# Kernel optimization log

Hardware: AMD Instinct MI355X
Metric: run time of the kernel (lower is better)

Reference implementation:

```python
import jax, jax.numpy as jnp
import numpy as np

N_NODES = 50000
N_EDGES = 800000
IN_CH, HID_CH, OUT_CH = 512, 512, 256


def setup_inputs() -> dict:
    key = jax.random.key(0)
    ks = jax.random.split(key, 8)
    x = jax.random.normal(ks[0], (N_NODES, IN_CH), dtype=jnp.float32)
    edge_index = jax.random.randint(ks[1], (2, N_EDGES), 0, N_NODES, dtype=jnp.int32)
    def glorot(k, fan_in, fan_out):
        s = jnp.sqrt(6.0 / (fan_in + fan_out))
        return jax.random.uniform(k, (fan_in, fan_out), jnp.float32, -s, s)
    W1 = glorot(ks[2], IN_CH, HID_CH)
    b1 = jnp.zeros((HID_CH,), jnp.float32)
    W2 = glorot(ks[3], HID_CH, HID_CH)
    b2 = jnp.zeros((HID_CH,), jnp.float32)
    W3 = glorot(ks[4], HID_CH, OUT_CH)
    b3 = jnp.zeros((OUT_CH,), jnp.float32)
    return {"x": x, "edge_index": edge_index, "W1": W1, "b1": b1,
            "W2": W2, "b2": b2, "W3": W3, "b3": b3}


def _gcn_conv(x, src, dst, W, b, n_nodes):
    """PyG GCNConv: add self-loops, symmetric deg^-1/2 normalization,
    linear transform, scatter-add aggregation, bias."""
    h = x @ W  # [N, out] dense transform first (in >= out)
    # degree counts include the self-loop (+1)
    deg = jax.ops.segment_sum(jnp.ones(src.shape, x.dtype), dst,
                              num_segments=n_nodes) + 1.0
    dinv = jax.lax.rsqrt(deg)  # [N]
    norm = dinv[src] * dinv[dst]  # [E]
    msg = h[src] * norm[:, None]  # [E, out]
    agg = jax.ops.segment_sum(msg, dst, num_segments=n_nodes)
    # self-loop contribution handled analytically: norm_ii = dinv[i]^2
    return agg + h * (dinv * dinv)[:, None] + b


def reference(x, edge_index, W1, b1, W2, b2, W3, b3):
    src, dst = edge_index[0], edge_index[1]
    n = x.shape[0]
    h = _gcn_conv(x, src, dst, W1, b1, n)
    h = jax.nn.gelu(h)  # dropout p=0.0 -> identity
    h = _gcn_conv(h, src, dst, W2, b2, n)
    h = jax.nn.gelu(h)
    out = _gcn_conv(h, src, dst, W3, b3, n)
    return out
```

## Files before the change

### kernel.cpp

```cpp
#include <hip/hip_runtime.h>
#include <hip/hip_fp16.h>
#include <math.h>

#define N_NODES 50000
#define N_EDGES 800000
#define MPAD 50048
#define NBANDS (MPAD / 128)
#define KPHYS 1024
#define KB 1024
#define NOUTER 16
#define SCANB ((N_NODES + 255) / 256)


__device__ __forceinline__ unsigned short bf16_rn(float f) {
    unsigned u = __float_as_uint(f);
    u += 0x7FFFu + ((u >> 16) & 1u);
    return (unsigned short)(u >> 16);
}
__device__ __forceinline__ float bf16_f32(unsigned short h) {
    return __uint_as_float(((unsigned)h) << 16);
}

typedef __attribute__((ext_vector_type(2))) float f2v;

__device__ __forceinline__ float2 ntload2(const float* p) {
    f2v v = __builtin_nontemporal_load((const f2v*)p);
    return make_float2(v[0], v[1]);
}


__global__ void zero_int_kernel(int* __restrict__ p, int n) {
    int i = blockIdx.x * blockDim.x + threadIdx.x;
    if (i < n) p[i] = 0;
}

__global__ void count_deg_kernel(const int* __restrict__ dst, int* __restrict__ deg) {
    int e = blockIdx.x * blockDim.x + threadIdx.x;
    if (e < N_EDGES) atomicAdd(&deg[dst[e]], 1);
}

__global__ void dinv_kernel(const int* __restrict__ deg, float* __restrict__ dinv) {
    int i = blockIdx.x * blockDim.x + threadIdx.x;
    if (i < N_NODES) dinv[i] = rsqrtf((float)deg[i] + 1.0f);
}

__global__ __launch_bounds__(256) void scan1_kernel(const int* __restrict__ deg,
                                                    int* __restrict__ local_scan,
                                                    int* __restrict__ partials) {
    __shared__ int sm[256];
    int b = blockIdx.x, t = threadIdx.x;
    int i = b * 256 + t;
    int v = (i < N_NODES) ? deg[i] : 0;
    sm[t] = v;
    __syncthreads();
    for (int off = 1; off < 256; off <<= 1) {
        int x = (t >= off) ? sm[t - off] : 0;
        __syncthreads();
        sm[t] += x;
        __syncthreads();
    }
    if (i < N_NODES) local_scan[i] = sm[t];
    if (t == 255) partials[b] = sm[255];
}

__global__ __launch_bounds__(256) void scan2_kernel(int* __restrict__ partials) {
    __shared__ int sm[256];
    int t = threadIdx.x;
    sm[t] = (t < SCANB) ? partials[t] : 0;
    __syncthreads();
    for (int off = 1; off < 256; off <<= 1) {
        int x = (t >= off) ? sm[t - off] : 0;
        __syncthreads();
        sm[t] += x;
        __syncthreads();
    }
    if (t < SCANB) partials[t] = (t == 0) ? 0 : sm[t - 1];
}

__global__ __launch_bounds__(256) void scan3_kernel(const int* __restrict__ deg,
                                                    const int* __restrict__ local_scan,
                                                    const int* __restrict__ partials,
                                                    int* __restrict__ offsets,
                                                    int* __restrict__ cursor) {
    int i = blockIdx.x * 256 + threadIdx.x;
    if (i == 0) offsets[0] = 0;
    if (i < N_NODES) {
        int incl = local_scan[i] + partials[blockIdx.x];
        offsets[i + 1] = incl;
        cursor[i] = incl - deg[i];
    }
}

__global__ void fill_csr_kernel(const int* __restrict__ src, const int* __restrict__ dst,
                                int* __restrict__ cursor, int2* __restrict__ csr_sw,
                                const float* __restrict__ dinv) {
    int e = blockIdx.x * blockDim.x + threadIdx.x;
    if (e < N_EDGES) {
        int s = src[e], d = dst[e];
        int p = atomicAdd(&cursor[d], 1);
        csr_sw[p] = make_int2(s, __float_as_int(dinv[s] * dinv[d]));
    }
}


typedef __attribute__((ext_vector_type(8))) short bf16x8;
typedef __attribute__((ext_vector_type(4))) float floatx4;

#define GLL16(g, l)                                                                   \
    __builtin_amdgcn_global_load_lds((__attribute__((address_space(1))) const void*)(g), \
                                     (__attribute__((address_space(3))) void*)(l), 16, 0, 0)

__global__ __launch_bounds__(256) void gemm_split_bt(const unsigned short* __restrict__ A2,
                                                     const unsigned short* __restrict__ B2T,
                                                     __half* __restrict__ Chi,
                                                     __half* __restrict__ Clo, int N,
                                                     int cshift) {
    const int b = blockIdx.x;
    const int xcd = b & 7;
    const int q = b >> 3;
    const int cb = q & ((1 << cshift) - 1);
    const int bh = q >> cshift;
    const int r = bh * 8 + xcd;
    if (r >= NBANDS) return;
    const int row0 = r * 128;
    const int col0 = cb * 128;

    __shared__ unsigned short As[2][2][128 * 32];
    __shared__ unsigned short Bs[2][2][128 * 32];

    const int t = threadIdx.x;
    const int lane = t & 63;
    const int quad = lane >> 4;
    const int l15 = lane & 15;
    const int w = t >> 6;
    const int wm = w & 1, wn = w >> 1;

    floatx4 acc[4][4];
#pragma unroll
    for (int i = 0; i < 4; i++)
#pragma unroll
        for (int j = 0; j < 4; j++) acc[i][j] = (floatx4){0.f, 0.f, 0.f, 0.f};

    const int sr = t >> 2;
    const int sk = ((t & 3) ^ ((t >> 3) & 3)) * 8;
    const unsigned short* Arow0 = A2 + (size_t)(row0 + sr) * KPHYS + sk;
    const unsigned short* Arow1 = Arow0 + (size_t)64 * KPHYS;
    const unsigned short* Brow0 = B2T + (size_t)(col0 + sr) * KB + sk;
    const unsigned short* Brow1 = Brow0 + (size_t)64 * KB;

    const int fcol = (quad ^ ((l15 >> 1) & 3)) * 8;

#define STAGE(buf, k32)                                            \
    do {                                                           \
        GLL16(Arow0 + (k32), As[buf][0] + t * 8);                  \
        GLL16(Arow1 + (k32), As[buf][0] + 2048 + t * 8);           \
        GLL16(Arow0 + 512 + (k32), As[buf][1] + t * 8);            \
        GLL16(Arow1 + 512 + (k32), As[buf][1] + 2048 + t * 8);     \
        GLL16(Brow0 + (k32), Bs[buf][0] + t * 8);                  \
        GLL16(Brow1 + (k32), Bs[buf][0] + 2048 + t * 8);           \
        GLL16(Brow0 + 512 + (k32), Bs[buf][1] + t * 8);            \
        GLL16(Brow1 + 512 + (k32), Bs[buf][1] + 2048 + t * 8);     \
    } while (0)

    STAGE(0, 0);

    for (int it = 0; it < NOUTER; it++) {
        const int cur = it & 1;
        __syncthreads();
        if (it + 1 < NOUTER) STAGE(cur ^ 1, (it + 1) * 32);

        bf16x8 afh[4], afl[4], bfh[4], bfl[4];
#pragma unroll
        for (int mt = 0; mt < 4; mt++) {
            const int ro = (wm * 64 + mt * 16 + l15) * 32 + fcol;
            afh[mt] = *(const bf16x8*)(As[cur][0] + ro);
            afl[mt] = *(const bf16x8*)(As[cur][1] + ro);
        }
#pragma unroll
        for (int nt = 0; nt < 4; nt++) {
            const int ro = (wn * 64 + nt * 16 + l15) * 32 + fcol;
            bfh[nt] = *(const bf16x8*)(Bs[cur][0] + ro);
            bfl[nt] = *(const bf16x8*)(Bs[cur][1] + ro);
        }
#pragma unroll
        for (int mt = 0; mt < 4; mt++)
#pragma unroll
            for (int nt = 0; nt < 4; nt++)
                acc[mt][nt] = __builtin_amdgcn_mfma_f32_16x16x32_bf16(afh[mt], bfh[nt], acc[mt][nt], 0, 0, 0);
#pragma unroll
        for (int mt = 0; mt < 4; mt++)
#pragma unroll
            for (int nt = 0; nt < 4; nt++)
                acc[mt][nt] = __builtin_amdgcn_mfma_f32_16x16x32_bf16(afl[mt], bfh[nt], acc[mt][nt], 0, 0, 0);
#pragma unroll
        for (int mt = 0; mt < 4; mt++)
#pragma unroll
            for (int nt = 0; nt < 4; nt++)
                acc[mt][nt] = __builtin_amdgcn_mfma_f32_16x16x32_bf16(afh[mt], bfl[nt], acc[mt][nt], 0, 0, 0);
    }
#undef STAGE

#pragma unroll
    for (int mt = 0; mt < 4; mt++) {
#pragma unroll
        for (int rr = 0; rr < 4; rr++) {
            int row = row0 + wm * 64 + mt * 16 + quad * 4 + rr;
            __half* Cph = Chi + (size_t)row * N + col0 + wn * 64 + l15;
            __half* Cpl = Clo + (size_t)row * N + col0 + wn * 64 + l15;
#pragma unroll
            for (int nt = 0; nt < 4; nt++) {
                float a = acc[mt][nt][rr];
                __half hi = __float2half(a);
                __half lo = __float2half(a - __half2float(hi));
                Cph[nt * 16] = hi;
                Cpl[nt * 16] = lo;
            }
        }
    }
}


__global__ void wsplit_kernel(const float* __restrict__ W, unsigned short* __restrict__ B2T, int N) {
    int idx = blockIdx.x * blockDim.x + threadIdx.x;
    if (idx >= 512 * N) return;
    int k = idx / N, n = idx % N;
    float v = W[(size_t)k * N + n];
    unsigned short hi = bf16_rn(v);
    unsigned short lo = bf16_rn(v - bf16_f32(hi));
    unsigned short* row = B2T + (size_t)n * KB;
    row[k] = hi;
    row[512 + k] = lo;
}


__global__ __launch_bounds__(256) void split_x_kernel(const float* __restrict__ x,
                                                      unsigned short* __restrict__ A2) {
    int m = blockIdx.x;
    int ch = threadIdx.x * 2;
    unsigned short* arow = A2 + (size_t)m * KPHYS;
    float vx = 0.f, vy = 0.f;
    if (m < N_NODES) {
        float2 v = ntload2(x + (size_t)m * 512 + ch);
        vx = v.x;
        vy = v.y;
    }
    unsigned short hx = bf16_rn(vx), hy = bf16_rn(vy);
    arow[ch] = hx;
    arow[ch + 1] = hy;
    arow[512 + ch] = bf16_rn(vx - bf16_f32(hx));
    arow[512 + ch + 1] = bf16_rn(vy - bf16_f32(hy));
}


__device__ __forceinline__ float gelu_tanh(float x) {
    float x3 = x * x * x;
    float inner = 0.7978845608028654f * (x + 0.044715f * x3);
    return 0.5f * x * (1.0f + tanhf(inner));
}

__global__ __launch_bounds__(256) void aggregate_split_kernel(
    const __half* __restrict__ Chi, const __half* __restrict__ Clo,
    const int* __restrict__ offsets, const int2* __restrict__ csr_sw,
    const float* __restrict__ dinv,
    const float* __restrict__ bias, unsigned short* __restrict__ A2) {
    int t = threadIdx.x;
    int node = __builtin_amdgcn_readfirstlane(blockIdx.x * 4 + (t >> 6));
    int ch = (t & 63) * 8;
    unsigned short* arow = A2 + (size_t)node * KPHYS;
    if (node >= N_NODES) {
        *(uint4*)(arow + ch) = make_uint4(0, 0, 0, 0);
        *(uint4*)(arow + 512 + ch) = make_uint4(0, 0, 0, 0);
        return;
    }
    int p0 = offsets[node], p1 = offsets[node + 1];
    float a[8] = {0.f, 0.f, 0.f, 0.f, 0.f, 0.f, 0.f, 0.f};

    union H8 { float4 f4; __half2 h2[4]; };
    int p = p0;
    int pend8 = p0 + ((p1 - p0) & ~7);
    for (; p < pend8; p += 8) {
        int2 e[8];
#pragma unroll
        for (int j = 0; j < 8; j++) e[j] = csr_sw[p + j];
        H8 v[8];
#pragma unroll
        for (int j = 0; j < 8; j++)
            v[j].f4 = *(const float4*)(Chi + (size_t)e[j].x * 512 + ch);
#pragma unroll
        for (int j = 0; j < 8; j++) {
            float wg = __int_as_float(e[j].y);
#pragma unroll
            for (int q = 0; q < 4; q++) {
                float2 c = __half22float2(v[j].h2[q]);
                a[2 * q] += wg * c.x;
                a[2 * q + 1] += wg * c.y;
            }
        }
    }
    if (p + 4 <= p1) {
        int2 e[4];
#pragma unroll
        for (int j = 0; j < 4; j++) e[j] = csr_sw[p + j];
        H8 v[4];
#pragma unroll
        for (int j = 0; j < 4; j++)
            v[j].f4 = *(const float4*)(Chi + (size_t)e[j].x * 512 + ch);
#pragma unroll
        for (int j = 0; j < 4; j++) {
            float wg = __int_as_float(e[j].y);
#pragma unroll
            for (int q = 0; q < 4; q++) {
                float2 c = __half22float2(v[j].h2[q]);
                a[2 * q] += wg * c.x;
                a[2 * q + 1] += wg * c.y;
            }
        }
        p += 4;
    }
    for (; p < p1; p++) {
        int2 e = csr_sw[p];
        float wg = __int_as_float(e.y);
        H8 v;
        v.f4 = *(const float4*)(Chi + (size_t)e.x * 512 + ch);
#pragma unroll
        for (int q = 0; q < 4; q++) {
            float2 c = __half22float2(v.h2[q]);
            a[2 * q] += wg * c.x;
            a[2 * q + 1] += wg * c.y;
        }
    }

    float di = dinv[node];
    float wself = di * di;
    H8 vh, vl;
    vh.f4 = *(const float4*)(Chi + (size_t)node * 512 + ch);
    vl.f4 = *(const float4*)(Clo + (size_t)node * 512 + ch);
    float4 bv0 = *(const float4*)(bias + ch);
    float4 bv1 = *(const float4*)(bias + ch + 4);
    float s[8], b[8] = {bv0.x, bv0.y, bv0.z, bv0.w, bv1.x, bv1.y, bv1.z, bv1.w};
#pragma unroll
    for (int j = 0; j < 4; j++) {
        float2 ch2 = __half22float2(vh.h2[j]);
        float2 cl2 = __half22float2(vl.h2[j]);
        s[2 * j] = ch2.x + cl2.x;
        s[2 * j + 1] = ch2.y + cl2.y;
    }

    unsigned short hi[8], lo[8];
#pragma unroll
    for (int j = 0; j < 8; j++) {
        float v = gelu_tanh(a[j] + wself * s[j] + b[j]);
        hi[j] = bf16_rn(v);
        lo[j] = bf16_rn(v - bf16_f32(hi[j]));
    }
    *(ushort4*)(arow + ch) = make_ushort4(hi[0], hi[1], hi[2], hi[3]);
    *(ushort4*)(arow + ch + 4) = make_ushort4(hi[4], hi[5], hi[6], hi[7]);
    *(ushort4*)(arow + 512 + ch) = make_ushort4(lo[0], lo[1], lo[2], lo[3]);
    *(ushort4*)(arow + 512 + ch + 4) = make_ushort4(lo[4], lo[5], lo[6], lo[7]);
}

__global__ __launch_bounds__(256) void aggregate_final_kernel(
    const __half* __restrict__ Chi, const __half* __restrict__ Clo,
    const int* __restrict__ offsets, const int2* __restrict__ csr_sw,
    const float* __restrict__ dinv,
    const float* __restrict__ bias, float* __restrict__ out) {
    int t = threadIdx.x;
    int node = __builtin_amdgcn_readfirstlane(blockIdx.x * 4 + (t >> 6));
    if (node >= N_NODES) return;
    int ch = (t & 63) * 4;
    int p0 = offsets[node], p1 = offsets[node + 1];
    float ax = 0.f, ay = 0.f, az = 0.f, aw = 0.f;

    union H4 { float2 f2; __half2 h2[2]; };
    int p = p0;
    int pend8 = p0 + ((p1 - p0) & ~7);
    for (; p < pend8; p += 8) {
        int2 e[8];
#pragma unroll
        for (int j = 0; j < 8; j++) e[j] = csr_sw[p + j];
        H4 v[8];
#pragma unroll
        for (int j = 0; j < 8; j++)
            v[j].f2 = *(const float2*)(Chi + (size_t)e[j].x * 256 + ch);
#pragma unroll
        for (int j = 0; j < 8; j++) {
            float wg = __int_as_float(e[j].y);
            float2 c0 = __half22float2(v[j].h2[0]), c1 = __half22float2(v[j].h2[1]);
            ax += wg * c0.x; ay += wg * c0.y; az += wg * c1.x; aw += wg * c1.y;
        }
    }
    for (; p < p1; p++) {
        int2 e = csr_sw[p];
        float wg = __int_as_float(e.y);
        H4 v;
        v.f2 = *(const float2*)(Chi + (size_t)e.x * 256 + ch);
        float2 c0 = __half22float2(v.h2[0]), c1 = __half22float2(v.h2[1]);
        ax += wg * c0.x; ay += wg * c0.y; az += wg * c1.x; aw += wg * c1.y;
    }

    float di = dinv[node];
    float wself = di * di;
    H4 vh, vl;
    vh.f2 = *(const float2*)(Chi + (size_t)node * 256 + ch);
    vl.f2 = *(const float2*)(Clo + (size_t)node * 256 + ch);
    float2 h0 = __half22float2(vh.h2[0]), h1 = __half22float2(vh.h2[1]);
    float2 l0 = __half22float2(vl.h2[0]), l1 = __half22float2(vl.h2[1]);
    float4 bv = *(const float4*)(bias + ch);
    float4 o = make_float4(ax + wself * (h0.x + l0.x) + bv.x,
                           ay + wself * (h0.y + l0.y) + bv.y,
                           az + wself * (h1.x + l1.x) + bv.z,
                           aw + wself * (h1.y + l1.y) + bv.w);
    *(float4*)(out + (size_t)node * 256 + ch) = o;
}


static inline char* align16(char* p) { return (char*)(((size_t)p + 15) & ~(size_t)15); }

extern "C" void kernel_launch(void* const* d_in, const int* in_sizes, int n_in,
                              void* d_out, int out_size, void* d_ws, size_t ws_size,
                              hipStream_t stream) {
    const float* x  = (const float*)d_in[0];
    const int* eidx = (const int*)d_in[1];
    const float* W1 = (const float*)d_in[2];
    const float* b1 = (const float*)d_in[3];
    const float* W2 = (const float*)d_in[4];
    const float* b2 = (const float*)d_in[5];
    const float* W3 = (const float*)d_in[6];
    const float* b3 = (const float*)d_in[7];
    float* out = (float*)d_out;

    const int* src = eidx;
    const int* dst = eidx + N_EDGES;

    char* ws = (char*)d_ws;
    unsigned short* A2 = (unsigned short*)ws;  ws += (size_t)MPAD * KPHYS * 2;
    __half* Chi = (__half*)ws;                 ws += (size_t)MPAD * 512 * 2;
    __half* Clo = (__half*)ws;                 ws += (size_t)MPAD * 512 * 2;
    unsigned short* B2T1 = (unsigned short*)ws; ws += (size_t)512 * KB * 2;
    unsigned short* B2T2 = (unsigned short*)ws; ws += (size_t)512 * KB * 2;
    unsigned short* B2T3 = (unsigned short*)ws; ws += (size_t)256 * KB * 2;
    int* deg = (int*)ws;        ws = align16(ws + (size_t)N_NODES * 4);
    float* dinv = (float*)ws;   ws = align16(ws + (size_t)N_NODES * 4);
    int* offsets = (int*)ws;    ws = align16(ws + (size_t)(N_NODES + 1) * 4);
    int* cursor = (int*)ws;     ws = align16(ws + (size_t)N_NODES * 4);
    int2* csr_sw = (int2*)ws;   ws = align16(ws + (size_t)N_EDGES * 8);
    int* local_scan = (int*)ws; ws = align16(ws + (size_t)N_NODES * 4);
    int* partials = (int*)ws;   ws = align16(ws + (size_t)SCANB * 4);

    zero_int_kernel<<<(N_NODES + 255) / 256, 256, 0, stream>>>(deg, N_NODES);
    count_deg_kernel<<<(N_EDGES + 255) / 256, 256, 0, stream>>>(dst, deg);
    dinv_kernel<<<(N_NODES + 255) / 256, 256, 0, stream>>>(deg, dinv);
    scan1_kernel<<<SCANB, 256, 0, stream>>>(deg, local_scan, partials);
    scan2_kernel<<<1, 256, 0, stream>>>(partials);
    scan3_kernel<<<SCANB, 256, 0, stream>>>(deg, local_scan, partials, offsets, cursor);
    fill_csr_kernel<<<(N_EDGES + 255) / 256, 256, 0, stream>>>(src, dst, cursor, csr_sw, dinv);

    wsplit_kernel<<<(512 * 512 + 255) / 256, 256, 0, stream>>>(W1, B2T1, 512);
    wsplit_kernel<<<(512 * 512 + 255) / 256, 256, 0, stream>>>(W2, B2T2, 512);
    wsplit_kernel<<<(512 * 256 + 255) / 256, 256, 0, stream>>>(W3, B2T3, 256);
    split_x_kernel<<<MPAD, 256, 0, stream>>>(x, A2);

    const int gemm_grid_512 = 8 * ((NBANDS + 7) / 8) * 4;
    const int gemm_grid_256 = 8 * ((NBANDS + 7) / 8) * 2;

    {
        gemm_split_bt<<<gemm_grid_512, 256, 0, stream>>>(A2, B2T1, Chi, Clo, 512, 2);
        aggregate_split_kernel<<<MPAD / 4, 256, 0, stream>>>(Chi, Clo, offsets, csr_sw, dinv, b1, A2);
    }
    {
        gemm_split_bt<<<gemm_grid_512, 256, 0, stream>>>(A2, B2T2, Chi, Clo, 512, 2);
        aggregate_split_kernel<<<MPAD / 4, 256, 0, stream>>>(Chi, Clo, offsets, csr_sw, dinv, b2, A2);
    }
    {
        gemm_split_bt<<<gemm_grid_256, 256, 0, stream>>>(A2, B2T3, Chi, Clo, 256, 1);
        aggregate_final_kernel<<<MPAD / 4, 256, 0, stream>>>(Chi, Clo, offsets, csr_sw, dinv, b3, out);
    }
}
```

Measured before the change: 883.5 us.

## Split aggregation across channel slices and edge-parallel lanes with shuffle reduction

Each aggregation block now handles one of eight channel slices for four nodes. Within a wavefront, lanes split the node's edge list (2 halves for the hidden layers, 4 groups for the final layer) and combine partial sums with cross-lane shuffles. Edge records are read with nontemporal loads. This multiplies the grid by eight and uses narrower 4-byte gathers, aiming at more memory-level parallelism on the irregular gathers. The cost is reading offsets, edges and dinv eight times per node, and lanes doing redundant epilogue work.

```diff
diff --git a/kernel.cpp b/kernel.cpp
--- a/kernel.cpp
+++ b/kernel.cpp
@@ -26,6 +26,11 @@
 __device__ __forceinline__ float2 ntload2(const float* p) {
     f2v v = __builtin_nontemporal_load((const f2v*)p);
     return make_float2(v[0], v[1]);
+}
+
+__device__ __forceinline__ int2 ntload_edge(const int2* p) {
+    long long raw = __builtin_nontemporal_load((const long long*)p);
+    return make_int2((int)(raw & 0xffffffffLL), (int)(raw >> 32));
 }
 
 
@@ -263,100 +268,72 @@
     const int* __restrict__ offsets, const int2* __restrict__ csr_sw,
     const float* __restrict__ dinv,
     const float* __restrict__ bias, unsigned short* __restrict__ A2) {
-    int t = threadIdx.x;
-    int node = __builtin_amdgcn_readfirstlane(blockIdx.x * 4 + (t >> 6));
-    int ch = (t & 63) * 8;
+    const int b = blockIdx.x;
+    const int slice = b & 7;
+    const int g = b >> 3;
+    const int t = threadIdx.x;
+    const int node = __builtin_amdgcn_readfirstlane(g * 4 + (t >> 6));
+    const int lane = t & 63;
+    const int half = lane >> 5;
+    const int ch = slice * 64 + (lane & 31) * 2;
+
     unsigned short* arow = A2 + (size_t)node * KPHYS;
     if (node >= N_NODES) {
-        *(uint4*)(arow + ch) = make_uint4(0, 0, 0, 0);
-        *(uint4*)(arow + 512 + ch) = make_uint4(0, 0, 0, 0);
+        if (half == 0) *(unsigned*)(arow + ch) = 0u;
+        else *(unsigned*)(arow + 512 + ch) = 0u;
         return;
     }
-    int p0 = offsets[node], p1 = offsets[node + 1];
-    float a[8] = {0.f, 0.f, 0.f, 0.f, 0.f, 0.f, 0.f, 0.f};
-
-    union H8 { float4 f4; __half2 h2[4]; };
-    int p = p0;
-    int pend8 = p0 + ((p1 - p0) & ~7);
-    for (; p < pend8; p += 8) {
-        int2 e[8];
-#pragma unroll
-        for (int j = 0; j < 8; j++) e[j] = csr_sw[p + j];
-        H8 v[8];
-#pragma unroll
-        for (int j = 0; j < 8; j++)
-            v[j].f4 = *(const float4*)(Chi + (size_t)e[j].x * 512 + ch);
-#pragma unroll
-        for (int j = 0; j < 8; j++) {
-            float wg = __int_as_float(e[j].y);
-#pragma unroll
-            for (int q = 0; q < 4; q++) {
-                float2 c = __half22float2(v[j].h2[q]);
-                a[2 * q] += wg * c.x;
-                a[2 * q + 1] += wg * c.y;
-            }
-        }
-    }
-    if (p + 4 <= p1) {
-        int2 e[4];
-#pragma unroll
-        for (int j = 0; j < 4; j++) e[j] = csr_sw[p + j];
-        H8 v[4];
-#pragma unroll
-        for (int j = 0; j < 4; j++)
-            v[j].f4 = *(const float4*)(Chi + (size_t)e[j].x * 512 + ch);
-#pragma unroll
-        for (int j = 0; j < 4; j++) {
-            float wg = __int_as_float(e[j].y);
-#pragma unroll
-            for (int q = 0; q < 4; q++) {
-                float2 c = __half22float2(v[j].h2[q]);
-                a[2 * q] += wg * c.x;
-                a[2 * q + 1] += wg * c.y;
-            }
-        }
-        p += 4;
-    }
-    for (; p < p1; p++) {
-        int2 e = csr_sw[p];
+
+    const int p0 = offsets[node], p1 = offsets[node + 1];
+    const int nedge = p1 - p0;
+    float a0 = 0.f, a1 = 0.f;
+
+    const int nfull = nedge & ~7;
+    int q = half;
+    for (; q < nfull; q += 8) {
+        int2 e0 = ntload_edge(csr_sw + p0 + q);
+        int2 e1 = ntload_edge(csr_sw + p0 + q + 2);
+        int2 e2 = ntload_edge(csr_sw + p0 + q + 4);
+        int2 e3 = ntload_edge(csr_sw + p0 + q + 6);
+        __half2 v0 = *(const __half2*)(Chi + (size_t)e0.x * 512 + ch);
+        __half2 v1 = *(const __half2*)(Chi + (size_t)e1.x * 512 + ch);
+        __half2 v2 = *(const __half2*)(Chi + (size_t)e2.x * 512 + ch);
+        __half2 v3 = *(const __half2*)(Chi + (size_t)e3.x * 512 + ch);
+        float2 c0 = __half22float2(v0), c1 = __half22float2(v1);
+        float2 c2 = __half22float2(v2), c3 = __half22float2(v3);
+        float w0 = __int_as_float(e0.y), w1 = __int_as_float(e1.y);
+        float w2 = __int_as_float(e2.y), w3 = __int_as_float(e3.y);
+        a0 += w0 * c0.x + w1 * c1.x + w2 * c2.x + w3 * c3.x;
+        a1 += w0 * c0.y + w1 * c1.y + w2 * c2.y + w3 * c3.y;
+    }
+    for (; q < nedge; q += 2) {
+        int2 e = ntload_edge(csr_sw + p0 + q);
+        __half2 v = *(const __half2*)(Chi + (size_t)e.x * 512 + ch);
+        float2 c = __half22float2(v);
         float wg = __int_as_float(e.y);
-        H8 v;
-        v.f4 = *(const float4*)(Chi + (size_t)e.x * 512 + ch);
-#pragma unroll
-        for (int q = 0; q < 4; q++) {
-            float2 c = __half22float2(v.h2[q]);
-            a[2 * q] += wg * c.x;
-            a[2 * q + 1] += wg * c.y;
-        }
-    }
+        a0 += wg * c.x;
+        a1 += wg * c.y;
+    }
+
+    a0 += __shfl_xor(a0, 32);
+    a1 += __shfl_xor(a1, 32);
 
     float di = dinv[node];
     float wself = di * di;
-    H8 vh, vl;
-    vh.f4 = *(const float4*)(Chi + (size_t)node * 512 + ch);
-    vl.f4 = *(const float4*)(Clo + (size_t)node * 512 + ch);
-    float4 bv0 = *(const float4*)(bias + ch);
-    float4 bv1 = *(const float4*)(bias + ch + 4);
-    float s[8], b[8] = {bv0.x, bv0.y, bv0.z, bv0.w, bv1.x, bv1.y, bv1.z, bv1.w};
-#pragma unroll
-    for (int j = 0; j < 4; j++) {
-        float2 ch2 = __half22float2(vh.h2[j]);
-        float2 cl2 = __half22float2(vl.h2[j]);
-        s[2 * j] = ch2.x + cl2.x;
-        s[2 * j + 1] = ch2.y + cl2.y;
-    }
-
-    unsigned short hi[8], lo[8];
-#pragma unroll
-    for (int j = 0; j < 8; j++) {
-        float v = gelu_tanh(a[j] + wself * s[j] + b[j]);
-        hi[j] = bf16_rn(v);
-        lo[j] = bf16_rn(v - bf16_f32(hi[j]));
-    }
-    *(ushort4*)(arow + ch) = make_ushort4(hi[0], hi[1], hi[2], hi[3]);
-    *(ushort4*)(arow + ch + 4) = make_ushort4(hi[4], hi[5], hi[6], hi[7]);
-    *(ushort4*)(arow + 512 + ch) = make_ushort4(lo[0], lo[1], lo[2], lo[3]);
-    *(ushort4*)(arow + 512 + ch + 4) = make_ushort4(lo[4], lo[5], lo[6], lo[7]);
+    __half2 vh = *(const __half2*)(Chi + (size_t)node * 512 + ch);
+    __half2 vl = *(const __half2*)(Clo + (size_t)node * 512 + ch);
+    float2 sh = __half22float2(vh), sl = __half22float2(vl);
+    float2 bv = *(const float2*)(bias + ch);
+    float r0 = gelu_tanh(a0 + wself * (sh.x + sl.x) + bv.x);
+    float r1 = gelu_tanh(a1 + wself * (sh.y + sl.y) + bv.y);
+
+    unsigned short h0 = bf16_rn(r0), h1 = bf16_rn(r1);
+    unsigned short l0 = bf16_rn(r0 - bf16_f32(h0)), l1 = bf16_rn(r1 - bf16_f32(h1));
+    if (half == 0) {
+        *(unsigned*)(arow + ch) = (unsigned)h0 | ((unsigned)h1 << 16);
+    } else {
+        *(unsigned*)(arow + 512 + ch) = (unsigned)l0 | ((unsigned)l1 << 16);
+    }
 }
 
 __global__ __launch_bounds__(256) void aggregate_final_kernel(
@@ -364,53 +341,57 @@
     const int* __restrict__ offsets, const int2* __restrict__ csr_sw,
     const float* __restrict__ dinv,
     const float* __restrict__ bias, float* __restrict__ out) {
-    int t = threadIdx.x;
-    int node = __builtin_amdgcn_readfirstlane(blockIdx.x * 4 + (t >> 6));
+    const int b = blockIdx.x;
+    const int slice = b & 7;
+    const int g = b >> 3;
+    const int t = threadIdx.x;
+    const int node = __builtin_amdgcn_readfirstlane(g * 4 + (t >> 6));
     if (node >= N_NODES) return;
-    int ch = (t & 63) * 4;
-    int p0 = offsets[node], p1 = offsets[node + 1];
-    float ax = 0.f, ay = 0.f, az = 0.f, aw = 0.f;
-
-    union H4 { float2 f2; __half2 h2[2]; };
-    int p = p0;
-    int pend8 = p0 + ((p1 - p0) & ~7);
-    for (; p < pend8; p += 8) {
-        int2 e[8];
-#pragma unroll
-        for (int j = 0; j < 8; j++) e[j] = csr_sw[p + j];
-        H4 v[8];
-#pragma unroll
-        for (int j = 0; j < 8; j++)
-            v[j].f2 = *(const float2*)(Chi + (size_t)e[j].x * 256 + ch);
-#pragma unroll
-        for (int j = 0; j < 8; j++) {
-            float wg = __int_as_float(e[j].y);
-            float2 c0 = __half22float2(v[j].h2[0]), c1 = __half22float2(v[j].h2[1]);
-            ax += wg * c0.x; ay += wg * c0.y; az += wg * c1.x; aw += wg * c1.y;
-        }
-    }
-    for (; p < p1; p++) {
-        int2 e = csr_sw[p];
+    const int lane = t & 63;
+    const int grp = lane >> 4;
+    const int ch = slice * 32 + (lane & 15) * 2;
+
+    const int p0 = offsets[node], p1 = offsets[node + 1];
+    const int nedge = p1 - p0;
+    float a0 = 0.f, a1 = 0.f;
+
+    const int nfull = nedge & ~7;
+    int q = grp;
+    for (; q < nfull; q += 8) {
+        int2 e0 = ntload_edge(csr_sw + p0 + q);
+        int2 e1 = ntload_edge(csr_sw + p0 + q + 4);
+        __half2 v0 = *(const __half2*)(Chi + (size_t)e0.x * 256 + ch);
+        __half2 v1 = *(const __half2*)(Chi + (size_t)e1.x * 256 + ch);
+        float2 c0 = __half22float2(v0), c1 = __half22float2(v1);
+        float w0 = __int_as_float(e0.y), w1 = __int_as_float(e1.y);
+        a0 += w0 * c0.x + w1 * c1.x;
+        a1 += w0 * c0.y + w1 * c1.y;
+    }
+    for (; q < nedge; q += 4) {
+        int2 e = ntload_edge(csr_sw + p0 + q);
+        __half2 v = *(const __half2*)(Chi + (size_t)e.x * 256 + ch);
+        float2 c = __half22float2(v);
         float wg = __int_as_float(e.y);
-        H4 v;
-        v.f2 = *(const float2*)(Chi + (size_t)e.x * 256 + ch);
-        float2 c0 = __half22float2(v.h2[0]), c1 = __half22float2(v.h2[1]);
-        ax += wg * c0.x; ay += wg * c0.y; az += wg * c1.x; aw += wg * c1.y;
-    }
+        a0 += wg * c.x;
+        a1 += wg * c.y;
+    }
+
+    a0 += __shfl_xor(a0, 16);
+    a1 += __shfl_xor(a1, 16);
+    a0 += __shfl_xor(a0, 32);
+    a1 += __shfl_xor(a1, 32);
 
     float di = dinv[node];
     float wself = di * di;
-    H4 vh, vl;
-    vh.f2 = *(const float2*)(Chi + (size_t)node * 256 + ch);
-    vl.f2 = *(const float2*)(Clo + (size_t)node * 256 + ch);
-    float2 h0 = __half22float2(vh.h2[0]), h1 = __half22float2(vh.h2[1]);
-    float2 l0 = __half22float2(vl.h2[0]), l1 = __half22float2(vl.h2[1]);
-    float4 bv = *(const float4*)(bias + ch);
-    float4 o = make_float4(ax + wself * (h0.x + l0.x) + bv.x,
-                           ay + wself * (h0.y + l0.y) + bv.y,
-                           az + wself * (h1.x + l1.x) + bv.z,
-                           aw + wself * (h1.y + l1.y) + bv.w);
-    *(float4*)(out + (size_t)node * 256 + ch) = o;
+    __half2 vh = *(const __half2*)(Chi + (size_t)node * 256 + ch);
+    __half2 vl = *(const __half2*)(Clo + (size_t)node * 256 + ch);
+    float2 sh = __half22float2(vh), sl = __half22float2(vl);
+    float2 bv = *(const float2*)(bias + ch);
+    if (lane < 16) {
+        float2 o = make_float2(a0 + wself * (sh.x + sl.x) + bv.x,
+                               a1 + wself * (sh.y + sl.y) + bv.y);
+        *(float2*)(out + (size_t)node * 256 + ch) = o;
+    }
 }
 
 
@@ -463,16 +444,19 @@
     const int gemm_grid_512 = 8 * ((NBANDS + 7) / 8) * 4;
     const int gemm_grid_256 = 8 * ((NBANDS + 7) / 8) * 2;
 
+    const int agg_grid = 8 * (MPAD / 4);
+    const int aggf_grid = 8 * ((N_NODES + 3) / 4);
+
     {
         gemm_split_bt<<<gemm_grid_512, 256, 0, stream>>>(A2, B2T1, Chi, Clo, 512, 2);
-        aggregate_split_kernel<<<MPAD / 4, 256, 0, stream>>>(Chi, Clo, offsets, csr_sw, dinv, b1, A2);
+        aggregate_split_kernel<<<agg_grid, 256, 0, stream>>>(Chi, Clo, offsets, csr_sw, dinv, b1, A2);
     }
     {
         gemm_split_bt<<<gemm_grid_512, 256, 0, stream>>>(A2, B2T2, Chi, Clo, 512, 2);
-        aggregate_split_kernel<<<MPAD / 4, 256, 0, stream>>>(Chi, Clo, offsets, csr_sw, dinv, b2, A2);
+        aggregate_split_kernel<<<agg_grid, 256, 0, stream>>>(Chi, Clo, offsets, csr_sw, dinv, b2, A2);
     }
     {
         gemm_split_bt<<<gemm_grid_256, 256, 0, stream>>>(A2, B2T3, Chi, Clo, 256, 1);
-        aggregate_final_kernel<<<MPAD / 4, 256, 0, stream>>>(Chi, Clo, offsets, csr_sw, dinv, b3, out);
-    }
-}
+        aggregate_final_kernel<<<aggf_grid, 256, 0, stream>>>(Chi, Clo, offsets, csr_sw, dinv, b3, out);
+    }
+}
```

Result: slower. 1.335 ms (+51.1%).

## Enlarge split-bf16 GEMM tiles to 256x256 with 512-thread blocks

Applied to the files above, without the earlier changes.

The split-precision GEMM moves from 128x128 tiles with 4 waves to 256x256 tiles with 8 waves (2x4 wave grid, 128x64 per wave). A fragments are now loaded per row tile inside the MFMA loop instead of all up front, which limits register pressure from the larger accumulator array. MPAD is padded to a multiple of 256 and the grid is shrunk to match. The goal is more reuse of each staged A/B tile and less global traffic per FLOP. In exchange, LDS per block doubles, occupancy and register headroom drop, and the grid has fewer blocks, so the GPU may be less evenly filled.

```diff
diff --git a/kernel.cpp b/kernel.cpp
--- a/kernel.cpp
+++ b/kernel.cpp
@@ -4,8 +4,8 @@
 
 #define N_NODES 50000
 #define N_EDGES 800000
-#define MPAD 50048
-#define NBANDS (MPAD / 128)
+#define MPAD 50176
+#define MT256 (MPAD / 256)
 #define KPHYS 1024
 #define KB 1024
 #define NOUTER 16
@@ -110,56 +110,56 @@
     __builtin_amdgcn_global_load_lds((__attribute__((address_space(1))) const void*)(g), \
                                      (__attribute__((address_space(3))) void*)(l), 16, 0, 0)
 
-__global__ __launch_bounds__(256) void gemm_split_bt(const unsigned short* __restrict__ A2,
-                                                     const unsigned short* __restrict__ B2T,
-                                                     __half* __restrict__ Chi,
-                                                     __half* __restrict__ Clo, int N,
-                                                     int cshift) {
+__global__ __launch_bounds__(512, 2) void gemm_split_bt(const unsigned short* __restrict__ A2,
+                                                        const unsigned short* __restrict__ B2T,
+                                                        __half* __restrict__ Chi,
+                                                        __half* __restrict__ Clo, int N,
+                                                        int cshift) {
     const int b = blockIdx.x;
     const int xcd = b & 7;
     const int q = b >> 3;
     const int cb = q & ((1 << cshift) - 1);
     const int bh = q >> cshift;
     const int r = bh * 8 + xcd;
-    if (r >= NBANDS) return;
-    const int row0 = r * 128;
-    const int col0 = cb * 128;
-
-    __shared__ unsigned short As[2][2][128 * 32];
-    __shared__ unsigned short Bs[2][2][128 * 32];
+    if (r >= MT256) return;
+    const int row0 = r * 256;
+    const int col0 = cb * 256;
+
+    __shared__ unsigned short As[2][2][256 * 32];
+    __shared__ unsigned short Bs[2][2][256 * 32];
 
     const int t = threadIdx.x;
     const int lane = t & 63;
     const int quad = lane >> 4;
     const int l15 = lane & 15;
     const int w = t >> 6;
-    const int wm = w & 1, wn = w >> 1;
-
-    floatx4 acc[4][4];
-#pragma unroll
-    for (int i = 0; i < 4; i++)
+    const int wm = w >> 2, wn = w & 3;
+
+    floatx4 acc[8][4];
+#pragma unroll
+    for (int i = 0; i < 8; i++)
 #pragma unroll
         for (int j = 0; j < 4; j++) acc[i][j] = (floatx4){0.f, 0.f, 0.f, 0.f};
 
     const int sr = t >> 2;
     const int sk = ((t & 3) ^ ((t >> 3) & 3)) * 8;
     const unsigned short* Arow0 = A2 + (size_t)(row0 + sr) * KPHYS + sk;
-    const unsigned short* Arow1 = Arow0 + (size_t)64 * KPHYS;
+    const unsigned short* Arow1 = Arow0 + (size_t)128 * KPHYS;
     const unsigned short* Brow0 = B2T + (size_t)(col0 + sr) * KB + sk;
-    const unsigned short* Brow1 = Brow0 + (size_t)64 * KB;
+    const unsigned short* Brow1 = Brow0 + (size_t)128 * KB;
 
     const int fcol = (quad ^ ((l15 >> 1) & 3)) * 8;
 
 #define STAGE(buf, k32)                                            \
     do {                                                           \
         GLL16(Arow0 + (k32), As[buf][0] + t * 8);                  \
-        GLL16(Arow1 + (k32), As[buf][0] + 2048 + t * 8);           \
+        GLL16(Arow1 + (k32), As[buf][0] + 4096 + t * 8);           \
         GLL16(Arow0 + 512 + (k32), As[buf][1] + t * 8);            \
-        GLL16(Arow1 + 512 + (k32), As[buf][1] + 2048 + t * 8);     \
+        GLL16(Arow1 + 512 + (k32), As[buf][1] + 4096 + t * 8);     \
         GLL16(Brow0 + (k32), Bs[buf][0] + t * 8);                  \
-        GLL16(Brow1 + (k32), Bs[buf][0] + 2048 + t * 8);           \
+        GLL16(Brow1 + (k32), Bs[buf][0] + 4096 + t * 8);           \
         GLL16(Brow0 + 512 + (k32), Bs[buf][1] + t * 8);            \
-        GLL16(Brow1 + 512 + (k32), Bs[buf][1] + 2048 + t * 8);     \
+        GLL16(Brow1 + 512 + (k32), Bs[buf][1] + 4096 + t * 8);     \
     } while (0)
 
     STAGE(0, 0);
@@ -169,13 +169,7 @@
         __syncthreads();
         if (it + 1 < NOUTER) STAGE(cur ^ 1, (it + 1) * 32);
 
-        bf16x8 afh[4], afl[4], bfh[4], bfl[4];
-#pragma unroll
-        for (int mt = 0; mt < 4; mt++) {
-            const int ro = (wm * 64 + mt * 16 + l15) * 32 + fcol;
-            afh[mt] = *(const bf16x8*)(As[cur][0] + ro);
-            afl[mt] = *(const bf16x8*)(As[cur][1] + ro);
-        }
+        bf16x8 bfh[4], bfl[4];
 #pragma unroll
         for (int nt = 0; nt < 4; nt++) {
             const int ro = (wn * 64 + nt * 16 + l15) * 32 + fcol;
@@ -183,28 +177,28 @@
             bfl[nt] = *(const bf16x8*)(Bs[cur][1] + ro);
         }
 #pragma unroll
-        for (int mt = 0; mt < 4; mt++)
+        for (int mt = 0; mt < 8; mt++) {
+            const int ro = (wm * 128 + mt * 16 + l15) * 32 + fcol;
+            bf16x8 ah = *(const bf16x8*)(As[cur][0] + ro);
+            bf16x8 al = *(const bf16x8*)(As[cur][1] + ro);
 #pragma unroll
             for (int nt = 0; nt < 4; nt++)
-                acc[mt][nt] = __builtin_amdgcn_mfma_f32_16x16x32_bf16(afh[mt], bfh[nt], acc[mt][nt], 0, 0, 0);
-#pragma unroll
-        for (int mt = 0; mt < 4; mt++)
+                acc[mt][nt] = __builtin_amdgcn_mfma_f32_16x16x32_bf16(ah, bfh[nt], acc[mt][nt], 0, 0, 0);
 #pragma unroll
             for (int nt = 0; nt < 4; nt++)
-                acc[mt][nt] = __builtin_amdgcn_mfma_f32_16x16x32_bf16(afl[mt], bfh[nt], acc[mt][nt], 0, 0, 0);
-#pragma unroll
-        for (int mt = 0; mt < 4; mt++)
+                acc[mt][nt] = __builtin_amdgcn_mfma_f32_16x16x32_bf16(al, bfh[nt], acc[mt][nt], 0, 0, 0);
 #pragma unroll
             for (int nt = 0; nt < 4; nt++)
-                acc[mt][nt] = __builtin_amdgcn_mfma_f32_16x16x32_bf16(afh[mt], bfl[nt], acc[mt][nt], 0, 0, 0);
+                acc[mt][nt] = __builtin_amdgcn_mfma_f32_16x16x32_bf16(ah, bfl[nt], acc[mt][nt], 0, 0, 0);
+        }
     }
 #undef STAGE
 
 #pragma unroll
-    for (int mt = 0; mt < 4; mt++) {
+    for (int mt = 0; mt < 8; mt++) {
 #pragma unroll
         for (int rr = 0; rr < 4; rr++) {
-            int row = row0 + wm * 64 + mt * 16 + quad * 4 + rr;
+            int row = row0 + wm * 128 + mt * 16 + quad * 4 + rr;
             __half* Cph = Chi + (size_t)row * N + col0 + wn * 64 + l15;
             __half* Cpl = Clo + (size_t)row * N + col0 + wn * 64 + l15;
 #pragma unroll
@@ -460,19 +454,19 @@
     wsplit_kernel<<<(512 * 256 + 255) / 256, 256, 0, stream>>>(W3, B2T3, 256);
     split_x_kernel<<<MPAD, 256, 0, stream>>>(x, A2);
 
-    const int gemm_grid_512 = 8 * ((NBANDS + 7) / 8) * 4;
-    const int gemm_grid_256 = 8 * ((NBANDS + 7) / 8) * 2;
+    const int gemm_grid_512 = 8 * ((MT256 + 7) / 8) * 2;
+    const int gemm_grid_256 = 8 * ((MT256 + 7) / 8) * 1;
 
     {
-        gemm_split_bt<<<gemm_grid_512, 256, 0, stream>>>(A2, B2T1, Chi, Clo, 512, 2);
+        gemm_split_bt<<<gemm_grid_512, 512, 0, stream>>>(A2, B2T1, Chi, Clo, 512, 1);
         aggregate_split_kernel<<<MPAD / 4, 256, 0, stream>>>(Chi, Clo, offsets, csr_sw, dinv, b1, A2);
     }
     {
-        gemm_split_bt<<<gemm_grid_512, 256, 0, stream>>>(A2, B2T2, Chi, Clo, 512, 2);
+        gemm_split_bt<<<gemm_grid_512, 512, 0, stream>>>(A2, B2T2, Chi, Clo, 512, 1);
         aggregate_split_kernel<<<MPAD / 4, 256, 0, stream>>>(Chi, Clo, offsets, csr_sw, dinv, b2, A2);
     }
     {
-        gemm_split_bt<<<gemm_grid_256, 256, 0, stream>>>(A2, B2T3, Chi, Clo, 256, 1);
+        gemm_split_bt<<<gemm_grid_256, 512, 0, stream>>>(A2, B2T3, Chi, Clo, 256, 0);
         aggregate_final_kernel<<<MPAD / 4, 256, 0, stream>>>(Chi, Clo, offsets, csr_sw, dinv, b3, out);
     }
 }
```

Result: faster. 863.0 us (-2.3%).
